# Kernel optimization log

Measured on AMD Instinct MI355X. Metric: run time of the kernel, lower is better.

The kernel has to match this reference:

```python
import jax, jax.numpy as jnp
import numpy as np

IMG_W = 256; IMG_H = 256; N_PTS = 320
MIN_DEPTH = 3.0; MAX_DEPTH = 9.0; NDC_EXTENT = 1.0
SCALING = 0.1; EA_EPS = 1e-10; NORM_EPS = 1e-8


def setup_inputs() -> dict:
    key = jax.random.key(0)
    B, D = 1, 256
    image3d = jax.random.uniform(key, (B, 1, D, D, D), dtype=jnp.float32)
    # PyTorch3D convention: X_cam = X_world @ R + T. Camera at z=-6 world looking at origin.
    R = jnp.tile(jnp.eye(3, dtype=jnp.float32)[None], (B, 1, 1))
    T = jnp.tile(jnp.array([[0.0, 0.0, 6.0]], dtype=jnp.float32), (B, 1))
    focal = jnp.full((B,), 1.7320508, dtype=jnp.float32)  # NDC focal, fov ~ 60deg
    return {"image3d": image3d, "R": R, "T": T, "focal": focal}


def _trilinear_sample(vol, pts):
    # vol: [C, D, H, W]; pts: [N, 3] in xyz order, normalized coords in [-1, 1]
    # (grid_sample semantics: align_corners=True, padding_mode='zeros')
    C, D, H, W = vol.shape
    sizes = jnp.array([W, H, D], dtype=pts.dtype)
    idx = (pts + 1.0) * 0.5 * (sizes - 1.0)
    i0f = jnp.floor(idx)
    frac = idx - i0f
    i0 = i0f.astype(jnp.int32)
    volf = vol.reshape(C, -1)
    out = jnp.zeros((C, pts.shape[0]), dtype=vol.dtype)
    for dz in (0, 1):
        for dy in (0, 1):
            for dx in (0, 1):
                ix = i0[:, 0] + dx; iy = i0[:, 1] + dy; iz = i0[:, 2] + dz
                w = ((frac[:, 0] if dx else 1.0 - frac[:, 0]) *
                     (frac[:, 1] if dy else 1.0 - frac[:, 1]) *
                     (frac[:, 2] if dz else 1.0 - frac[:, 2]))
                valid = (ix >= 0) & (ix < W) & (iy >= 0) & (iy < H) & (iz >= 0) & (iz < D)
                lin = (jnp.clip(iz, 0, D - 1) * H + jnp.clip(iy, 0, H - 1)) * W + jnp.clip(ix, 0, W - 1)
                out = out + jnp.where(valid, w, 0.0)[None, :] * volf[:, lin]
    return out


def reference(image3d, R, T, focal):
    B, Cin, D, H, W = image3d.shape
    # features = image3d.repeat(1,3,1,1,1) when single channel
    features = jnp.broadcast_to(image3d, (B, 3, D, H, W)) if Cin == 1 else image3d
    densities = jnp.ones_like(image3d[:, :1]) * SCALING  # [B,1,D,H,W]
    shape = max(Cin, D)
    voxel_size = 2.0 * NDC_EXTENT / shape
    # Volumes local coords: world extent voxel_size*(size-1) maps to [-1,1]
    half_extent = jnp.array([voxel_size * (W - 1) / 2.0,
                             voxel_size * (H - 1) / 2.0,
                             voxel_size * (D - 1) / 2.0], dtype=image3d.dtype)
    # NDC pixel-center grid (PyTorch3D: +x left, +y up)
    xs = jnp.linspace(1.0 - 1.0 / IMG_W, -(1.0 - 1.0 / IMG_W), IMG_W, dtype=image3d.dtype)
    ys = jnp.linspace(1.0 - 1.0 / IMG_H, -(1.0 - 1.0 / IMG_H), IMG_H, dtype=image3d.dtype)
    depths = jnp.linspace(MIN_DEPTH, MAX_DEPTH, N_PTS, dtype=image3d.dtype)
    gy, gx = jnp.meshgrid(ys, xs, indexing="ij")  # [Hi, Wi]
    f = focal[:, None, None, None]
    dd = depths[None, None, None, :]
    x_cam = gx[None, :, :, None] * dd / f
    y_cam = gy[None, :, :, None] * dd / f
    z_cam = jnp.broadcast_to(dd, x_cam.shape)
    pts_cam = jnp.stack([x_cam, y_cam, z_cam], axis=-1)  # [B, Hi, Wi, P, 3]
    # unproject: X_world = (X_cam - T) @ R^T, i.e. X_world_i = sum_j (Xc - T)_j R_ij
    pts_world = jnp.einsum('bhwpj,bij->bhwpi', pts_cam - T[:, None, None, None, :], R)
    pts_local = pts_world / half_extent
    vol = jnp.concatenate([features, densities], axis=1)  # [B, 4, D, H, W]
    N = IMG_H * IMG_W * N_PTS
    vals = jax.vmap(_trilinear_sample)(vol, pts_local.reshape(B, N, 3))  # [B, 4, N]
    vals = vals.reshape(B, 4, IMG_H, IMG_W, N_PTS)
    feats = vals[:, :3]           # [B, 3, Hi, Wi, P]
    dens = vals[:, 3]             # [B, Hi, Wi, P]
    # EmissionAbsorption raymarcher: shifted cumprod absorption, alpha compositing
    cp = jnp.cumprod((1.0 + EA_EPS) - dens, axis=-1)
    absorption = jnp.concatenate([jnp.ones_like(cp[..., :1]), cp[..., :-1]], axis=-1)
    weights = dens * absorption
    rgb = jnp.einsum('bhwp,bchwp->bhwc', weights, feats)      # [B, Hi, Wi, 3]
    opacity = 1.0 - jnp.prod(1.0 - dens, axis=-1)             # [B, Hi, Wi]
    rgba = jnp.concatenate([rgb, opacity[..., None]], axis=-1)  # [B, Hi, Wi, 4]
    screen = jnp.transpose(rgba, (0, 3, 2, 1))                # [B, 4, Wi, Hi]
    gray = screen.mean(axis=1, keepdims=True)                 # is_grayscale=True
    return (gray + NORM_EPS) / (gray.max() + NORM_EPS)        # minimized()
```

## Files before the change

kernel.cpp:

```cpp
#include <hip/hip_runtime.h>

#define IMG_W 256
#define IMG_H 256
#define N_PTS 320
#define VD 256
#define VH 256
#define VW 256
#define DSTEP (6.0f / (N_PTS - 1))
#define RPB 16
#define CPR 16


struct RayCoef { float fAx, fBx, fAy, fBy, fAz, fBz; };

__device__ __forceinline__ RayCoef ray_coef(int w, int h,
                                            const float* __restrict__ Rm,
                                            const float* __restrict__ Tv,
                                            const float* __restrict__ focal) {
    const float a  = 1.0f - 1.0f / IMG_W;
    const float gx = a - (2.0f * a / (IMG_W - 1)) * (float)w;
    const float gy = a - (2.0f * a / (IMG_H - 1)) * (float)h;
    const float f  = focal[0];
    const float ux = gx / f, uy = gy / f;
    const float R00 = Rm[0], R01 = Rm[1], R02 = Rm[2];
    const float R10 = Rm[3], R11 = Rm[4], R12 = Rm[5];
    const float R20 = Rm[6], R21 = Rm[7], R22 = Rm[8];
    const float Tx = Tv[0], Ty = Tv[1], Tz = Tv[2];
    const float Bx = R00 * ux + R01 * uy + R02;
    const float By = R10 * ux + R11 * uy + R12;
    const float Bz = R20 * ux + R21 * uy + R22;
    const float Ax = -(R00 * Tx + R01 * Ty + R02 * Tz);
    const float Ay = -(R10 * Tx + R11 * Ty + R12 * Tz);
    const float Az = -(R20 * Tx + R21 * Ty + R22 * Tz);
    const float voxel = 2.0f / 256.0f;
    const float hx = voxel * (VW - 1) * 0.5f;
    const float hy = voxel * (VH - 1) * 0.5f;
    const float hz = voxel * (VD - 1) * 0.5f;
    const float sxc = 0.5f * (VW - 1) / hx, oxc = 0.5f * (VW - 1);
    const float syc = 0.5f * (VH - 1) / hy, oyc = 0.5f * (VH - 1);
    const float szc = 0.5f * (VD - 1) / hz, ozc = 0.5f * (VD - 1);
    RayCoef rc;
    rc.fBx = Bx * sxc; rc.fAx = Ax * sxc + oxc;
    rc.fBy = By * syc; rc.fAy = Ay * syc + oyc;
    rc.fBz = Bz * szc; rc.fAz = Az * szc + ozc;
    return rc;
}

__device__ __forceinline__ void clip_ray(const RayCoef& rc, int& pmin, int& len) {
    float dlo = 3.0f, dhi = 9.0f;
    const float lo = -1.0f, hi = 256.0f;
    const float fA[3] = { rc.fAx, rc.fAy, rc.fAz };
    const float fB[3] = { rc.fBx, rc.fBy, rc.fBz };
    #pragma unroll
    for (int dim = 0; dim < 3; ++dim) {
        if (fabsf(fB[dim]) > 1e-12f) {
            const float r = 1.0f / fB[dim];
            const float t0 = (lo - fA[dim]) * r, t1 = (hi - fA[dim]) * r;
            dlo = fmaxf(dlo, fminf(t0, t1));
            dhi = fminf(dhi, fmaxf(t0, t1));
        } else if (fA[dim] < lo || fA[dim] >= hi) {
            dhi = -1.0f;
        }
    }
    pmin = 0; len = 0;
    if (dhi > dlo) {
        pmin = max(0, (int)floorf((dlo - 3.0f) / DSTEP) - 1);
        int pmax = min(N_PTS, (int)ceilf((dhi - 3.0f) / DSTEP) + 2);
        len = max(0, pmax - pmin);
    }
}

__global__ __launch_bounds__(256) void prep_kernel(
    const float* __restrict__ Rm, const float* __restrict__ Tv,
    const float* __restrict__ focal, float* __restrict__ out,
    unsigned int* __restrict__ wsu)
{
    const int w = threadIdx.x;
    const int h = blockIdx.x;
    const RayCoef rc = ray_coef(w, h, Rm, Tv, focal);
    int pmin, len;
    clip_ray(rc, pmin, len);

    const bool active = (len > 0);
    if (!active) out[w * IMG_H + h] = 0.0f;

    const unsigned long long mask = __ballot(active);
    const int lane = threadIdx.x & 63;
    const int cnt  = __popcll(mask);
    if (cnt) {
        const int leader = __ffsll(mask) - 1;
        unsigned int base = 0;
        if (lane == leader) base = atomicAdd(&wsu[1], (unsigned)cnt);
        base = __shfl(base, leader);
        if (active) {
            const int rank = __popcll(mask & ((1ull << lane) - 1ull));
            uint2 e;
            e.x = (unsigned)(h * IMG_W + w) | ((unsigned)pmin << 16);
            e.y = (unsigned)len;
            ((uint2*)(wsu + 2))[base + rank] = e;
        }
    }
}

__global__ __launch_bounds__(256) void render_kernel(
    const float* __restrict__ vol, const float* __restrict__ Rm,
    const float* __restrict__ Tv, const float* __restrict__ focal,
    float* __restrict__ out, unsigned int* __restrict__ wsu)
{
    const unsigned count = wsu[1];
    if (blockIdx.x * RPB >= count) return;

    const int tx = threadIdx.x;
    const int ty = threadIdx.y;
    const unsigned slot = blockIdx.x * RPB + tx;
    const bool valid = (slot < count);

    uint2 e = make_uint2(0u, 0u);
    if (valid) e = ((const uint2*)(wsu + 2))[slot];
    const int rayid = (int)(e.x & 0xffffu);
    const int pmin  = (int)(e.x >> 16);
    const int len   = (int)e.y;
    const int w = rayid & (IMG_W - 1);
    const int h = rayid >> 8;

    const RayCoef rc = ray_coef(w, h, Rm, Tv, focal);

    const int plo = pmin + ((len * ty) >> 4);
    const int phi = pmin + ((len * (ty + 1)) >> 4);

    float S = 0.0f, A = 1.0f;
    for (int p = plo; p < phi; ++p) {
        const float d = 3.0f + (float)p * DSTEP;
        const float fx = fmaf(rc.fBx, d, rc.fAx);
        const float fy = fmaf(rc.fBy, d, rc.fAy);
        const float fz = fmaf(rc.fBz, d, rc.fAz);

        const float flx = floorf(fx), fly = floorf(fy), flz = floorf(fz);
        const int ix0 = (int)flx, iy0 = (int)fly, iz0 = (int)flz;

        float dens = 0.0f, feat = 0.0f;
        if (ix0 >= -1 && ix0 < VW && iy0 >= -1 && iy0 < VH && iz0 >= -1 && iz0 < VD) {
            const float frx = fx - flx, fry = fy - fly, frz = fz - flz;
            float wx0 = 1.0f - frx, wx1 = frx;
            float wy0 = 1.0f - fry, wy1 = fry;
            float wz0 = 1.0f - frz, wz1 = frz;
            if (ix0 < 0)       wx0 = 0.0f;
            if (ix0 + 1 >= VW) wx1 = 0.0f;
            if (iy0 < 0)       wy0 = 0.0f;
            if (iy0 + 1 >= VH) wy1 = 0.0f;
            if (iz0 < 0)       wz0 = 0.0f;
            if (iz0 + 1 >= VD) wz1 = 0.0f;

            const int cx0 = max(ix0, 0), cx1 = min(ix0 + 1, VW - 1);
            const int cy0 = max(iy0, 0), cy1 = min(iy0 + 1, VH - 1);
            const int cz0 = max(iz0, 0), cz1 = min(iz0 + 1, VD - 1);

            const int zb0 = cz0 * (VH * VW), zb1 = cz1 * (VH * VW);
            const int yb0 = cy0 * VW,        yb1 = cy1 * VW;

            const float v000 = vol[zb0 + yb0 + cx0];
            const float v001 = vol[zb0 + yb0 + cx1];
            const float v010 = vol[zb0 + yb1 + cx0];
            const float v011 = vol[zb0 + yb1 + cx1];
            const float v100 = vol[zb1 + yb0 + cx0];
            const float v101 = vol[zb1 + yb0 + cx1];
            const float v110 = vol[zb1 + yb1 + cx0];
            const float v111 = vol[zb1 + yb1 + cx1];

            const float w00 = wy0 * wz0, w01 = wy1 * wz0;
            const float w10 = wy0 * wz1, w11 = wy1 * wz1;
            const float c000 = wx0 * w00, c001 = wx1 * w00;
            const float c010 = wx0 * w01, c011 = wx1 * w01;
            const float c100 = wx0 * w10, c101 = wx1 * w10;
            const float c110 = wx0 * w11, c111 = wx1 * w11;

            feat = c000 * v000 + c001 * v001 + c010 * v010 + c011 * v011
                 + c100 * v100 + c101 * v101 + c110 * v110 + c111 * v111;
            dens = 0.1f * (c000 + c001 + c010 + c011 + c100 + c101 + c110 + c111);
        }

        S = fmaf(dens * A, feat, S);
        A *= (1.0f - dens);
    }

    __shared__ float lS[CPR][RPB];
    __shared__ float lA[CPR][RPB];
    lS[ty][tx] = S;
    lA[ty][tx] = A;
    __syncthreads();

    if (ty == 0) {
        float Stot = 0.0f, Atot = 1.0f;
        #pragma unroll
        for (int c = 0; c < CPR; ++c) {
            Stot = fmaf(Atot, lS[c][tx], Stot);
            Atot *= lA[c][tx];
        }
        const float gray = (3.0f * Stot + (1.0f - Atot)) * 0.25f;
        if (valid) out[w * IMG_H + h] = gray;

        float m = valid ? gray : 0.0f;
        m = fmaxf(m, __shfl_down(m, 8));
        m = fmaxf(m, __shfl_down(m, 4));
        m = fmaxf(m, __shfl_down(m, 2));
        m = fmaxf(m, __shfl_down(m, 1));
        if (tx == 0 && m > 0.0f)
            atomicMax(&wsu[0], __float_as_uint(m));
    }
}

__global__ __launch_bounds__(256) void normalize_kernel(
    float* __restrict__ out, const unsigned int* __restrict__ wsu)
{
    const int i = blockIdx.x * blockDim.x + threadIdx.x;
    const float m = __uint_as_float(wsu[0]);
    out[i] = (out[i] + 1e-8f) / (m + 1e-8f);
}

extern "C" void kernel_launch(void* const* d_in, const int* in_sizes, int n_in,
                              void* d_out, int out_size, void* d_ws, size_t ws_size,
                              hipStream_t stream) {
    (void)in_sizes; (void)n_in; (void)out_size; (void)ws_size;
    const float* vol   = (const float*)d_in[0];
    const float* Rm    = (const float*)d_in[1];
    const float* Tv    = (const float*)d_in[2];
    const float* focal = (const float*)d_in[3];
    float* out = (float*)d_out;
    unsigned int* wsu = (unsigned int*)d_ws;

    hipMemsetAsync(d_ws, 0, 8, stream);

    prep_kernel<<<IMG_H, IMG_W, 0, stream>>>(Rm, Tv, focal, out, wsu);

    dim3 rblock(RPB, CPR, 1);
    dim3 rgrid((IMG_W * IMG_H + RPB - 1) / RPB, 1, 1);
    render_kernel<<<rgrid, rblock, 0, stream>>>(vol, Rm, Tv, focal, out, wsu);

    normalize_kernel<<<(IMG_W * IMG_H) / 256, 256, 0, stream>>>(out, wsu);
}
```

Before: 108.7 us.

## Drop ray-compaction prep pass and atomics; use per-block max partials

```diff
diff --git a/kernel.cpp b/kernel.cpp
--- a/kernel.cpp
+++ b/kernel.cpp
@@ -9,6 +9,7 @@
 #define DSTEP (6.0f / (N_PTS - 1))
 #define RPB 16
 #define CPR 16
+#define NBLK ((IMG_W / RPB) * IMG_H)
 
 
 struct RayCoef { float fAx, fBx, fAy, fBy, fAz, fBz; };
@@ -70,60 +71,19 @@
     }
 }
 
-__global__ __launch_bounds__(256) void prep_kernel(
-    const float* __restrict__ Rm, const float* __restrict__ Tv,
-    const float* __restrict__ focal, float* __restrict__ out,
-    unsigned int* __restrict__ wsu)
+__global__ __launch_bounds__(256) void render_kernel(
+    const float* __restrict__ vol, const float* __restrict__ Rm,
+    const float* __restrict__ Tv, const float* __restrict__ focal,
+    float* __restrict__ out, float* __restrict__ wsf)
 {
-    const int w = threadIdx.x;
-    const int h = blockIdx.x;
+    const int tx = threadIdx.x;
+    const int ty = threadIdx.y;
+    const int w = blockIdx.x * RPB + tx;
+    const int h = blockIdx.y;
+
     const RayCoef rc = ray_coef(w, h, Rm, Tv, focal);
     int pmin, len;
     clip_ray(rc, pmin, len);
-
-    const bool active = (len > 0);
-    if (!active) out[w * IMG_H + h] = 0.0f;
-
-    const unsigned long long mask = __ballot(active);
-    const int lane = threadIdx.x & 63;
-    const int cnt  = __popcll(mask);
-    if (cnt) {
-        const int leader = __ffsll(mask) - 1;
-        unsigned int base = 0;
-        if (lane == leader) base = atomicAdd(&wsu[1], (unsigned)cnt);
-        base = __shfl(base, leader);
-        if (active) {
-            const int rank = __popcll(mask & ((1ull << lane) - 1ull));
-            uint2 e;
-            e.x = (unsigned)(h * IMG_W + w) | ((unsigned)pmin << 16);
-            e.y = (unsigned)len;
-            ((uint2*)(wsu + 2))[base + rank] = e;
-        }
-    }
-}
-
-__global__ __launch_bounds__(256) void render_kernel(
-    const float* __restrict__ vol, const float* __restrict__ Rm,
-    const float* __restrict__ Tv, const float* __restrict__ focal,
-    float* __restrict__ out, unsigned int* __restrict__ wsu)
-{
-    const unsigned count = wsu[1];
-    if (blockIdx.x * RPB >= count) return;
-
-    const int tx = threadIdx.x;
-    const int ty = threadIdx.y;
-    const unsigned slot = blockIdx.x * RPB + tx;
-    const bool valid = (slot < count);
-
-    uint2 e = make_uint2(0u, 0u);
-    if (valid) e = ((const uint2*)(wsu + 2))[slot];
-    const int rayid = (int)(e.x & 0xffffu);
-    const int pmin  = (int)(e.x >> 16);
-    const int len   = (int)e.y;
-    const int w = rayid & (IMG_W - 1);
-    const int h = rayid >> 8;
-
-    const RayCoef rc = ray_coef(w, h, Rm, Tv, focal);
 
     const int plo = pmin + ((len * ty) >> 4);
     const int phi = pmin + ((len * (ty + 1)) >> 4);
@@ -197,24 +157,43 @@
             Atot *= lA[c][tx];
         }
         const float gray = (3.0f * Stot + (1.0f - Atot)) * 0.25f;
-        if (valid) out[w * IMG_H + h] = gray;
-
-        float m = valid ? gray : 0.0f;
+        out[w * IMG_H + h] = gray;
+
+        float m = gray;
         m = fmaxf(m, __shfl_down(m, 8));
         m = fmaxf(m, __shfl_down(m, 4));
         m = fmaxf(m, __shfl_down(m, 2));
         m = fmaxf(m, __shfl_down(m, 1));
-        if (tx == 0 && m > 0.0f)
-            atomicMax(&wsu[0], __float_as_uint(m));
+        if (tx == 0)
+            wsf[blockIdx.y * (IMG_W / RPB) + blockIdx.x] = m;
     }
 }
 
 __global__ __launch_bounds__(256) void normalize_kernel(
-    float* __restrict__ out, const unsigned int* __restrict__ wsu)
+    float* __restrict__ out, const float* __restrict__ wsf)
 {
-    const int i = blockIdx.x * blockDim.x + threadIdx.x;
-    const float m = __uint_as_float(wsu[0]);
-    out[i] = (out[i] + 1e-8f) / (m + 1e-8f);
+    __shared__ float smax[4];
+    const int t = threadIdx.x;
+
+    float m = 0.0f;
+    const float4* v4 = (const float4*)wsf;
+    #pragma unroll
+    for (int k = 0; k < 4; ++k) {
+        const float4 v = v4[t + 256 * k];
+        m = fmaxf(m, fmaxf(fmaxf(v.x, v.y), fmaxf(v.z, v.w)));
+    }
+    m = fmaxf(m, __shfl_down(m, 32));
+    m = fmaxf(m, __shfl_down(m, 16));
+    m = fmaxf(m, __shfl_down(m, 8));
+    m = fmaxf(m, __shfl_down(m, 4));
+    m = fmaxf(m, __shfl_down(m, 2));
+    m = fmaxf(m, __shfl_down(m, 1));
+    if ((t & 63) == 0) smax[t >> 6] = m;
+    __syncthreads();
+    const float mm = fmaxf(fmaxf(smax[0], smax[1]), fmaxf(smax[2], smax[3]));
+
+    const int i = blockIdx.x * 256 + t;
+    out[i] = (out[i] + 1e-8f) / (mm + 1e-8f);
 }
 
 extern "C" void kernel_launch(void* const* d_in, const int* in_sizes, int n_in,
@@ -226,15 +205,11 @@
     const float* Tv    = (const float*)d_in[2];
     const float* focal = (const float*)d_in[3];
     float* out = (float*)d_out;
-    unsigned int* wsu = (unsigned int*)d_ws;
-
-    hipMemsetAsync(d_ws, 0, 8, stream);
-
-    prep_kernel<<<IMG_H, IMG_W, 0, stream>>>(Rm, Tv, focal, out, wsu);
+    float* wsf = (float*)d_ws;
 
     dim3 rblock(RPB, CPR, 1);
-    dim3 rgrid((IMG_W * IMG_H + RPB - 1) / RPB, 1, 1);
-    render_kernel<<<rgrid, rblock, 0, stream>>>(vol, Rm, Tv, focal, out, wsu);
-
-    normalize_kernel<<<(IMG_W * IMG_H) / 256, 256, 0, stream>>>(out, wsu);
-}
+    dim3 rgrid(IMG_W / RPB, IMG_H, 1);
+    render_kernel<<<rgrid, rblock, 0, stream>>>(vol, Rm, Tv, focal, out, wsf);
+
+    normalize_kernel<<<(IMG_W * IMG_H) / 256, 256, 0, stream>>>(out, wsf);
+}
```

New measurement: 109.6 us. Within noise of the previous version (+0.8%).
